# Optimization experiments

Measured on AMD Instinct MI355X. Metric: run time of the kernel, lower is better.

## Reference

```python
import jax, jax.numpy as jnp
import numpy as np

B, N, DIM = 4, 4096, 1024
HEADS, DIM_HEAD = 16, 64
DIM_INNER = HEADS * DIM_HEAD
ATTN_SCALE = 8.0
EPS = 1e-12  # F.normalize default eps


def setup_inputs() -> dict:
    key = jax.random.key(0)
    k1, k2, k3, k4, k5 = jax.random.split(key, 5)
    x = jax.random.normal(k1, (B, N, DIM), dtype=jnp.float32)
    gamma = jnp.ones((DIM,), dtype=jnp.float32)
    # stored as (in, out) so forward is x @ w
    w_qkv = jax.random.normal(k2, (DIM, 3 * DIM_INNER), dtype=jnp.float32) * (DIM ** -0.5)
    temperature = jnp.ones((HEADS, 1, 1), dtype=jnp.float32)
    w_out = jax.random.normal(k3, (DIM_INNER, DIM), dtype=jnp.float32) * (DIM_INNER ** -0.5)
    return {"x": x, "gamma": gamma, "w_qkv": w_qkv, "temperature": temperature, "w_out": w_out}


def _l2norm(t):
    # F.normalize(t, dim=-1): t / max(||t||_2, eps)
    n = jnp.linalg.norm(t, axis=-1, keepdims=True)
    return t / jnp.maximum(n, EPS)


def reference(x, gamma, w_qkv, temperature, w_out):
    b, n, dim = x.shape
    # RMSNorm: F.normalize(x, dim=-1) * sqrt(dim) * gamma
    xn = _l2norm(x) * (dim ** 0.5) * gamma
    # QKV projection -> qkv b h d n
    qkv = (xn @ w_qkv).reshape(b, n, 3, HEADS, DIM_HEAD)
    qkv = qkv.transpose(2, 0, 3, 4, 1)  # (3, b, h, d, n)
    q, k, v = qkv[0], qkv[1], qkv[2]
    # l2-normalize q, k over the sequence (last) axis; temperature-scale q
    q = _l2norm(q) * jnp.exp(temperature)  # temperature: (h,1,1) broadcast
    k = _l2norm(k)
    # cross-covariance attention over the small channel dim d
    sim = jnp.einsum('bhdn,bhen->bhde', q, k) * ATTN_SCALE
    attn = jax.nn.softmax(sim, axis=-1)
    out = jnp.einsum('bhde,bhen->bhdn', attn, v)
    # b h d n -> b n (h d), then out projection
    out = out.transpose(0, 3, 1, 2).reshape(b, n, DIM_INNER)
    return out @ w_out
```

## Files before the change

### kernel.cpp

```cpp
#include <hip/hip_runtime.h>
#include <stdint.h>

typedef unsigned short u16;
typedef unsigned int u32;
typedef __attribute__((ext_vector_type(8))) __bf16 bf16x8;
typedef __attribute__((ext_vector_type(4))) float f32x4;

#define M_TOT 16384
#define DIMX  1024

__device__ __forceinline__ u16 f2b(float f) {
  u32 u = __builtin_bit_cast(u32, f);
  u32 r = (u + 0x7fffu + ((u >> 16) & 1u)) >> 16;
  return (u16)r;
}

__device__ __forceinline__ void gl2lds16(const void* g, void* l) {
  __builtin_amdgcn_global_load_lds((const __attribute__((address_space(1))) void*)g,
                                   (__attribute__((address_space(3))) void*)l,
                                   16, 0, 0);
}

__global__ __launch_bounds__(256) void k_rms(const float* __restrict__ x,
                                             const float* __restrict__ gamma,
                                             u16* __restrict__ xn) {
  int row = blockIdx.x;
  int t = threadIdx.x;
  const float4* xr = (const float4*)(x + (size_t)row * DIMX);
  float4 v = xr[t];
  float ss = v.x * v.x + v.y * v.y + v.z * v.z + v.w * v.w;
#pragma unroll
  for (int o = 32; o > 0; o >>= 1) ss += __shfl_xor(ss, o, 64);
  __shared__ float wss[4];
  int w = t >> 6;
  if ((t & 63) == 0) wss[w] = ss;
  __syncthreads();
  float tot = wss[0] + wss[1] + wss[2] + wss[3];
  float scale = 32.0f / fmaxf(sqrtf(tot), 1e-12f);
  float4 g = ((const float4*)gamma)[t];
  ushort4 o4;
  o4.x = f2b(v.x * scale * g.x);
  o4.y = f2b(v.y * scale * g.y);
  o4.z = f2b(v.z * scale * g.z);
  o4.w = f2b(v.w * scale * g.w);
  ((ushort4*)xn)[(size_t)row * 256 + t] = o4;
}

__global__ __launch_bounds__(256) void k_castT(const float* __restrict__ in,
                                               u16* __restrict__ out, int Rr, int Cc) {
  __shared__ float tile[32][33];
  int c0 = blockIdx.x * 32, r0 = blockIdx.y * 32;
  int tx = threadIdx.x, ty = threadIdx.y;
#pragma unroll
  for (int i = 0; i < 4; i++)
    tile[ty + i * 8][tx] = in[(size_t)(r0 + ty + i * 8) * Cc + c0 + tx];
  __syncthreads();
#pragma unroll
  for (int i = 0; i < 4; i++)
    out[(size_t)(c0 + ty + i * 8) * Rr + r0 + tx] = f2b(tile[tx][ty + i * 8]);
}


template<bool SWAP>
__device__ __forceinline__ f32x4 mf(bf16x8 a, bf16x8 b, f32x4 c) {
  return SWAP ? __builtin_amdgcn_mfma_f32_16x16x32_bf16(b, a, c, 0, 0, 0)
              : __builtin_amdgcn_mfma_f32_16x16x32_bf16(a, b, c, 0, 0, 0);
}

__device__ __forceinline__ void stage_half(const u16* __restrict__ g,
                                           u16* dst, int t, int k0) {
#pragma unroll
  for (int r = 0; r < 2; r++) {
    int chunk = r * 512 + t;
    int row = chunk >> 3;
    int cc = (chunk & 7) ^ (row & 7);
    gl2lds16(g + (size_t)row * 1024 + (k0 + cc * 8),
             dst + (r * 512 + (t >> 6) * 64) * 8);
  }
}

template<bool SWAP>
__device__ __forceinline__ void gemm_core256(const u16* __restrict__ Ag,
                                             const u16* __restrict__ Bg,
                                             u16* lds, int t, f32x4 (&acc)[8][4]) {
  const int lane = t & 63;
  const int r16 = lane & 15, q = lane >> 4;
  const int wr = (t >> 6) >> 2, wc = (t >> 6) & 3;
  const int s0 = (q ^ (r16 & 7)) * 8;
  const int arow = wr * 16 + r16;
  const int brow = wc * 16 + r16;

  stage_half(Ag,              lds + 0 * 8192, t, 0);
  stage_half(Bg,              lds + 2 * 8192, t, 0);
  stage_half(Bg + 128 * 1024, lds + 3 * 8192, t, 0);
  stage_half(Ag + 128 * 1024, lds + 1 * 8192, t, 0);
  asm volatile("s_waitcnt vmcnt(4)" ::: "memory");
  __builtin_amdgcn_s_barrier();

  bf16x8 af[4][2], bl[2][2], bh[2][2];
#pragma unroll 1
  for (int tt = 0; tt < 16; tt++) {
    const int bo = (tt & 1) << 15;
    const int nb = bo ^ 32768;
    const int k1 = ((tt + 1) & 15) << 6;
    const u16* A0 = lds + bo;
    const u16* A1 = lds + bo + 8192;
    const u16* B0 = lds + bo + 16384;
    const u16* B1 = lds + bo + 24576;

#pragma unroll
    for (int i = 0; i < 4; i++) {
      af[i][0] = *(const bf16x8*)(A0 + (i * 32 + arow) * 64 + s0);
      af[i][1] = *(const bf16x8*)(A0 + (i * 32 + arow) * 64 + (s0 ^ 32));
    }
#pragma unroll
    for (int j = 0; j < 2; j++) {
      bl[j][0] = *(const bf16x8*)(B0 + (j * 64 + brow) * 64 + s0);
      bl[j][1] = *(const bf16x8*)(B0 + (j * 64 + brow) * 64 + (s0 ^ 32));
    }
    stage_half(Ag, lds + nb + 0 * 8192, t, k1);
    asm volatile("s_waitcnt lgkmcnt(8)" ::: "memory");
    __builtin_amdgcn_s_barrier();
    asm volatile("s_waitcnt lgkmcnt(0)" ::: "memory");
    __builtin_amdgcn_s_setprio(1);
#pragma unroll
    for (int kq = 0; kq < 2; kq++)
#pragma unroll
      for (int i = 0; i < 4; i++)
#pragma unroll
        for (int j = 0; j < 2; j++)
          acc[i][j] = mf<SWAP>(af[i][kq], bl[j][kq], acc[i][j]);
    __builtin_amdgcn_s_setprio(0);
    asm volatile("s_waitcnt vmcnt(4)" ::: "memory");
    __builtin_amdgcn_s_barrier();

#pragma unroll
    for (int j = 0; j < 2; j++) {
      bh[j][0] = *(const bf16x8*)(B1 + (j * 64 + brow) * 64 + s0);
      bh[j][1] = *(const bf16x8*)(B1 + (j * 64 + brow) * 64 + (s0 ^ 32));
    }
    stage_half(Bg, lds + nb + 2 * 8192, t, k1);
    __builtin_amdgcn_s_barrier();
    asm volatile("s_waitcnt lgkmcnt(0)" ::: "memory");
    __builtin_amdgcn_s_setprio(1);
#pragma unroll
    for (int kq = 0; kq < 2; kq++)
#pragma unroll
      for (int i = 0; i < 4; i++)
#pragma unroll
        for (int j = 0; j < 2; j++)
          acc[i][2 + j] = mf<SWAP>(af[i][kq], bh[j][kq], acc[i][2 + j]);
    __builtin_amdgcn_s_setprio(0);
    asm volatile("s_waitcnt vmcnt(4)" ::: "memory");
    __builtin_amdgcn_s_barrier();

#pragma unroll
    for (int i = 0; i < 4; i++) {
      af[i][0] = *(const bf16x8*)(A1 + (i * 32 + arow) * 64 + s0);
      af[i][1] = *(const bf16x8*)(A1 + (i * 32 + arow) * 64 + (s0 ^ 32));
    }
    stage_half(Bg + 128 * 1024, lds + nb + 3 * 8192, t, k1);
    __builtin_amdgcn_s_barrier();
    asm volatile("s_waitcnt lgkmcnt(0)" ::: "memory");
    __builtin_amdgcn_s_setprio(1);
#pragma unroll
    for (int kq = 0; kq < 2; kq++)
#pragma unroll
      for (int i = 0; i < 4; i++)
#pragma unroll
        for (int j = 0; j < 2; j++)
          acc[4 + i][j] = mf<SWAP>(af[i][kq], bl[j][kq], acc[4 + i][j]);
    __builtin_amdgcn_s_setprio(0);
    __builtin_amdgcn_s_barrier();

    stage_half(Ag + 128 * 1024, lds + nb + 1 * 8192, t, k1);
    __builtin_amdgcn_s_barrier();
    __builtin_amdgcn_s_setprio(1);
#pragma unroll
    for (int kq = 0; kq < 2; kq++)
#pragma unroll
      for (int i = 0; i < 4; i++)
#pragma unroll
        for (int j = 0; j < 2; j++)
          acc[4 + i][2 + j] = mf<SWAP>(af[i][kq], bh[j][kq], acc[4 + i][2 + j]);
    __builtin_amdgcn_s_setprio(0);
    asm volatile("s_waitcnt vmcnt(4)" ::: "memory");
    __builtin_amdgcn_s_barrier();
  }
}

__global__ __launch_bounds__(512, 2) void k_gemm1(const u16* __restrict__ A,
                                                  const u16* __restrict__ Bt,
                                                  u16* __restrict__ qkT,
                                                  u16* __restrict__ vmat,
                                                  float* __restrict__ sumsq) {
  __shared__ u16 lds[8 * 8192];
  int l = blockIdx.x;
  int wg = (l & 7) * 96 + (l >> 3);
  int mt = wg & 63, nt = wg >> 6;
  int m0 = mt * 256, n0 = nt * 256;
  int t = threadIdx.x, lane = t & 63;
  int r16 = lane & 15, q = lane >> 4;
  int wr = (t >> 6) >> 2, wc = (t >> 6) & 3;
  f32x4 acc[8][4] = {};
  if (n0 < 2048) {
    gemm_core256<false>(A + (size_t)m0 * 1024, Bt + (size_t)n0 * 1024, lds, t, acc);
    int b = m0 >> 12;
#pragma unroll
    for (int j = 0; j < 4; j++) {
      int c = n0 + j * 64 + wc * 16 + r16;
      float colss = 0.f;
#pragma unroll
      for (int i = 0; i < 8; i++) {
        f32x4 a = acc[i][j];
        colss += a.x * a.x + a.y * a.y + a.z * a.z + a.w * a.w;
        int m = m0 + i * 32 + wr * 16 + q * 4;
        ushort4 o4;
        o4.x = f2b(a.x); o4.y = f2b(a.y); o4.z = f2b(a.z); o4.w = f2b(a.w);
        *(ushort4*)(qkT + (size_t)c * M_TOT + m) = o4;
      }
      colss += __shfl_xor(colss, 16, 64);
      colss += __shfl_xor(colss, 32, 64);
      if (lane < 16) atomicAdd(&sumsq[b * 2048 + c], colss);
    }
  } else {
    gemm_core256<true>(A + (size_t)m0 * 1024, Bt + (size_t)n0 * 1024, lds, t, acc);
    int vc0 = n0 - 2048;
#pragma unroll
    for (int i = 0; i < 8; i++) {
      int m = m0 + i * 32 + wr * 16 + r16;
#pragma unroll
      for (int j = 0; j < 4; j++) {
        int c = vc0 + j * 64 + wc * 16 + q * 4;
        f32x4 a = acc[i][j];
        ushort4 o4;
        o4.x = f2b(a.x); o4.y = f2b(a.y); o4.z = f2b(a.z); o4.w = f2b(a.w);
        *(ushort4*)(vmat + (size_t)m * 1024 + c) = o4;
      }
    }
  }
}

__global__ __launch_bounds__(256) void k_attn_s(const u16* __restrict__ qkT,
                                                float* __restrict__ Spart) {
  int g = blockIdx.x, split = blockIdx.y;
  int t = threadIdx.x, lane = t & 63, w = t >> 6;
  int bh = g * 4 + w;
  int b = bh >> 4, h = bh & 15;
  int r16 = lane & 15, q = lane >> 4;
  const u16* qbase = qkT + (size_t)(h * 64) * M_TOT + b * 4096;
  const u16* kbase = qkT + (size_t)(1024 + h * 64) * M_TOT + b * 4096;
  f32x4 acc[4][4] = {};
#pragma unroll
  for (int it = 0; it < 8; it++) {
    int kk = split * 256 + it * 32 + q * 8;
    bf16x8 af[4], bfr[4];
#pragma unroll
    for (int i = 0; i < 4; i++) af[i] = *(const bf16x8*)(qbase + (size_t)(i * 16 + r16) * M_TOT + kk);
#pragma unroll
    for (int j = 0; j < 4; j++) bfr[j] = *(const bf16x8*)(kbase + (size_t)(j * 16 + r16) * M_TOT + kk);
#pragma unroll
    for (int i = 0; i < 4; i++)
#pragma unroll
      for (int j = 0; j < 4; j++)
        acc[i][j] = __builtin_amdgcn_mfma_f32_16x16x32_bf16(bfr[j], af[i], acc[i][j], 0, 0, 0);
  }
  float* Sp = Spart + ((size_t)split * 64 + bh) * 4096;
#pragma unroll
  for (int i = 0; i < 4; i++) {
    int d = i * 16 + r16;
#pragma unroll
    for (int j = 0; j < 4; j++) {
      int e = j * 16 + q * 4;
      *(f32x4*)(Sp + d * 64 + e) = acc[i][j];
    }
  }
}

__global__ __launch_bounds__(64) void k_softmax(const float* __restrict__ Spart,
                                                const float* __restrict__ sumsq,
                                                const float* __restrict__ temp,
                                                u16* __restrict__ PT) {
  int bh = blockIdx.x;
  int b = bh >> 4, h = bh & 15;
  int d = threadIdx.x;
  __shared__ float rnk[64];
  rnk[d] = 1.0f / fmaxf(sqrtf(sumsq[b * 2048 + 1024 + h * 64 + d]), 1e-12f);
  __syncthreads();
  float nq = sqrtf(sumsq[b * 2048 + h * 64 + d]);
  float qs = 8.0f * __expf(temp[h]) / fmaxf(nq, 1e-12f);
  const float* Sp = Spart + (size_t)bh * 4096 + d * 64;
  float vals[64];
#pragma unroll
  for (int e = 0; e < 64; e += 4) {
    f32x4 v = {};
#pragma unroll
    for (int s = 0; s < 16; s++)
      v += *(const f32x4*)(Sp + (size_t)s * 64 * 4096 + e);
    vals[e + 0] = v.x; vals[e + 1] = v.y; vals[e + 2] = v.z; vals[e + 3] = v.w;
  }
  float mx = -3.0e38f;
#pragma unroll
  for (int e = 0; e < 64; e++) {
    float v = vals[e] * qs * rnk[e];
    vals[e] = v;
    mx = fmaxf(mx, v);
  }
  float sum = 0.f;
#pragma unroll
  for (int e = 0; e < 64; e++) {
    float v = __expf(vals[e] - mx);
    vals[e] = v;
    sum += v;
  }
  float inv = 1.0f / sum;
#pragma unroll
  for (int e = 0; e < 64; e++)
    PT[((size_t)bh * 64 + e) * 64 + d] = f2b(vals[e] * inv);
}

__global__ __launch_bounds__(256) void k_m(const u16* __restrict__ woT,
                                           const u16* __restrict__ PT,
                                           u16* __restrict__ MT) {
  int bh = blockIdx.x;
  int b = bh >> 4, h = bh & 15;
  int o0 = blockIdx.y * 128;
  int t = threadIdx.x, lane = t & 63, w = t >> 6;
  int r16 = lane & 15, q = lane >> 4;
  const u16* pbase = PT + (size_t)bh * 4096;
  f32x4 acc[2][4] = {};
#pragma unroll
  for (int ks = 0; ks < 2; ks++) {
    int kk = ks * 32 + q * 8;
    bf16x8 af[2], bfr[4];
#pragma unroll
    for (int i = 0; i < 2; i++)
      af[i] = *(const bf16x8*)(woT + (size_t)(o0 + w * 32 + i * 16 + r16) * 1024 + h * 64 + kk);
#pragma unroll
    for (int j = 0; j < 4; j++)
      bfr[j] = *(const bf16x8*)(pbase + (size_t)(j * 16 + r16) * 64 + kk);
#pragma unroll
    for (int i = 0; i < 2; i++)
#pragma unroll
      for (int j = 0; j < 4; j++)
        acc[i][j] = __builtin_amdgcn_mfma_f32_16x16x32_bf16(af[i], bfr[j], acc[i][j], 0, 0, 0);
  }
  u16* dst = MT + (size_t)b * 1024 * 1024;
#pragma unroll
  for (int i = 0; i < 2; i++) {
    int o = o0 + w * 32 + i * 16 + q * 4;
#pragma unroll
    for (int j = 0; j < 4; j++) {
      int e = h * 64 + j * 16 + r16;
      f32x4 a = acc[i][j];
      dst[(size_t)(o + 0) * 1024 + e] = f2b(a.x);
      dst[(size_t)(o + 1) * 1024 + e] = f2b(a.y);
      dst[(size_t)(o + 2) * 1024 + e] = f2b(a.z);
      dst[(size_t)(o + 3) * 1024 + e] = f2b(a.w);
    }
  }
}

__global__ __launch_bounds__(512, 2) void k_gemm2(const u16* __restrict__ A,
                                                  const u16* __restrict__ Bt,
                                                  float* __restrict__ C) {
  __shared__ u16 lds[8 * 8192];
  int l = blockIdx.x;
  int wg = (l & 7) * 32 + (l >> 3);
  int mt = wg & 63, nt = wg >> 6;
  int m0 = mt * 256, n0 = nt * 256;
  int b = m0 >> 12;
  const u16* Bb = Bt + (size_t)b * 1024 * 1024;
  int t = threadIdx.x, lane = t & 63;
  int r16 = lane & 15, q = lane >> 4;
  int wr = (t >> 6) >> 2, wc = (t >> 6) & 3;
  f32x4 acc[8][4] = {};
  gemm_core256<true>(A + (size_t)m0 * 1024, Bb + (size_t)n0 * 1024, lds, t, acc);
#pragma unroll
  for (int i = 0; i < 8; i++) {
    int m = m0 + i * 32 + wr * 16 + r16;
#pragma unroll
    for (int j = 0; j < 4; j++) {
      int c = n0 + j * 64 + wc * 16 + q * 4;
      *(f32x4*)(C + (size_t)m * 1024 + c) = acc[i][j];
    }
  }
}

extern "C" void kernel_launch(void* const* d_in, const int* in_sizes, int n_in,
                              void* d_out, int out_size, void* d_ws, size_t ws_size,
                              hipStream_t stream) {
  const float* x     = (const float*)d_in[0];
  const float* gamma = (const float*)d_in[1];
  const float* wqkv  = (const float*)d_in[2];
  const float* temp  = (const float*)d_in[3];
  const float* wout  = (const float*)d_in[4];
  float* out = (float*)d_out;

  char* ws = (char*)d_ws;
  size_t off = 0;
  u16* xn = (u16*)(ws + off);    off += (size_t)M_TOT * 1024 * 2;
  u16* wqT = (u16*)(ws + off);   off += (size_t)3072 * 1024 * 2;
  u16* woT = (u16*)(ws + off);   off += (size_t)1024 * 1024 * 2;
  u16* qkT = (u16*)(ws + off);   off += (size_t)2048 * M_TOT * 2;
  u16* vmat = (u16*)(ws + off);  off += (size_t)M_TOT * 1024 * 2;
  float* sumsq = (float*)(ws + off); off += (size_t)4 * 2048 * 4;
  u16* PT = (u16*)(ws + off);    off += (size_t)64 * 64 * 64 * 2;
  u16* MT = (u16*)(ws + off);    off += (size_t)4 * 1024 * 1024 * 2;

  float* Spart = (float*)xn;

  hipMemsetAsync((void*)sumsq, 0, (size_t)4 * 2048 * 4, stream);

  k_rms<<<16384, 256, 0, stream>>>(x, gamma, xn);
  dim3 cb(32, 8);
  k_castT<<<dim3(3072 / 32, 1024 / 32), cb, 0, stream>>>(wqkv, wqT, 1024, 3072);
  k_castT<<<dim3(1024 / 32, 1024 / 32), cb, 0, stream>>>(wout, woT, 1024, 1024);
  k_gemm1<<<768, 512, 0, stream>>>(xn, wqT, qkT, vmat, sumsq);
  k_attn_s<<<dim3(16, 16), 256, 0, stream>>>(qkT, Spart);
  k_softmax<<<64, 64, 0, stream>>>(Spart, sumsq, temp, PT);
  k_m<<<dim3(64, 8), 256, 0, stream>>>(woT, PT, MT);
  k_gemm2<<<1024 / 4, 512, 0, stream>>>(vmat, MT, out);
}
```

Baseline: 338.0 us.

## Drop intra-iteration barriers in GEMM core and remap tiles per XCD

Removes several workgroup barriers and explicit LDS waitcnts between the async stage issue and the MFMA phases in the 256x256 GEMM main loop. One barrier with a vmcnt wait is kept per phase boundary. This cuts synchronisation stalls so waves can overlap LDS reads, staging and MFMA more freely. Both GEMMs also change their block-to-tile mapping so each XCD gets 8 consecutive M tiles, which should improve L2 reuse of the A operand. Fewer barriers risk LDS read/write races if the remaining waits do not cover every hazard.

```diff
diff --git a/kernel.cpp b/kernel.cpp
--- a/kernel.cpp
+++ b/kernel.cpp
@@ -119,9 +119,6 @@
       bl[j][1] = *(const bf16x8*)(B0 + (j * 64 + brow) * 64 + (s0 ^ 32));
     }
     stage_half(Ag, lds + nb + 0 * 8192, t, k1);
-    asm volatile("s_waitcnt lgkmcnt(8)" ::: "memory");
-    __builtin_amdgcn_s_barrier();
-    asm volatile("s_waitcnt lgkmcnt(0)" ::: "memory");
     __builtin_amdgcn_s_setprio(1);
 #pragma unroll
     for (int kq = 0; kq < 2; kq++)
@@ -140,8 +137,6 @@
       bh[j][1] = *(const bf16x8*)(B1 + (j * 64 + brow) * 64 + (s0 ^ 32));
     }
     stage_half(Bg, lds + nb + 2 * 8192, t, k1);
-    __builtin_amdgcn_s_barrier();
-    asm volatile("s_waitcnt lgkmcnt(0)" ::: "memory");
     __builtin_amdgcn_s_setprio(1);
 #pragma unroll
     for (int kq = 0; kq < 2; kq++)
@@ -160,8 +155,6 @@
       af[i][1] = *(const bf16x8*)(A1 + (i * 32 + arow) * 64 + (s0 ^ 32));
     }
     stage_half(Bg + 128 * 1024, lds + nb + 3 * 8192, t, k1);
-    __builtin_amdgcn_s_barrier();
-    asm volatile("s_waitcnt lgkmcnt(0)" ::: "memory");
     __builtin_amdgcn_s_setprio(1);
 #pragma unroll
     for (int kq = 0; kq < 2; kq++)
@@ -174,7 +167,6 @@
     __builtin_amdgcn_s_barrier();
 
     stage_half(Ag + 128 * 1024, lds + nb + 1 * 8192, t, k1);
-    __builtin_amdgcn_s_barrier();
     __builtin_amdgcn_s_setprio(1);
 #pragma unroll
     for (int kq = 0; kq < 2; kq++)
@@ -196,8 +188,9 @@
                                                   float* __restrict__ sumsq) {
   __shared__ u16 lds[8 * 8192];
   int l = blockIdx.x;
-  int wg = (l & 7) * 96 + (l >> 3);
-  int mt = wg & 63, nt = wg >> 6;
+  int xcd = l & 7, c = l >> 3;
+  int mt = xcd * 8 + (c & 7);
+  int nt = c >> 3;
   int m0 = mt * 256, n0 = nt * 256;
   int t = threadIdx.x, lane = t & 63;
   int r16 = lane & 15, q = lane >> 4;
@@ -208,7 +201,7 @@
     int b = m0 >> 12;
 #pragma unroll
     for (int j = 0; j < 4; j++) {
-      int c = n0 + j * 64 + wc * 16 + r16;
+      int cc = n0 + j * 64 + wc * 16 + r16;
       float colss = 0.f;
 #pragma unroll
       for (int i = 0; i < 8; i++) {
@@ -217,11 +210,11 @@
         int m = m0 + i * 32 + wr * 16 + q * 4;
         ushort4 o4;
         o4.x = f2b(a.x); o4.y = f2b(a.y); o4.z = f2b(a.z); o4.w = f2b(a.w);
-        *(ushort4*)(qkT + (size_t)c * M_TOT + m) = o4;
+        *(ushort4*)(qkT + (size_t)cc * M_TOT + m) = o4;
       }
       colss += __shfl_xor(colss, 16, 64);
       colss += __shfl_xor(colss, 32, 64);
-      if (lane < 16) atomicAdd(&sumsq[b * 2048 + c], colss);
+      if (lane < 16) atomicAdd(&sumsq[b * 2048 + cc], colss);
     }
   } else {
     gemm_core256<true>(A + (size_t)m0 * 1024, Bt + (size_t)n0 * 1024, lds, t, acc);
@@ -231,11 +224,11 @@
       int m = m0 + i * 32 + wr * 16 + r16;
 #pragma unroll
       for (int j = 0; j < 4; j++) {
-        int c = vc0 + j * 64 + wc * 16 + q * 4;
+        int cc = vc0 + j * 64 + wc * 16 + q * 4;
         f32x4 a = acc[i][j];
         ushort4 o4;
         o4.x = f2b(a.x); o4.y = f2b(a.y); o4.z = f2b(a.z); o4.w = f2b(a.w);
-        *(ushort4*)(vmat + (size_t)m * 1024 + c) = o4;
+        *(ushort4*)(vmat + (size_t)m * 1024 + cc) = o4;
       }
     }
   }
@@ -366,8 +359,9 @@
                                                   float* __restrict__ C) {
   __shared__ u16 lds[8 * 8192];
   int l = blockIdx.x;
-  int wg = (l & 7) * 32 + (l >> 3);
-  int mt = wg & 63, nt = wg >> 6;
+  int xcd = l & 7, c = l >> 3;
+  int mt = xcd * 8 + (c & 7);
+  int nt = c >> 3;
   int m0 = mt * 256, n0 = nt * 256;
   int b = m0 >> 12;
   const u16* Bb = Bt + (size_t)b * 1024 * 1024;
@@ -381,8 +375,8 @@
     int m = m0 + i * 32 + wr * 16 + r16;
 #pragma unroll
     for (int j = 0; j < 4; j++) {
-      int c = n0 + j * 64 + wc * 16 + q * 4;
-      *(f32x4*)(C + (size_t)m * 1024 + c) = acc[i][j];
+      int cc = n0 + j * 64 + wc * 16 + q * 4;
+      *(f32x4*)(C + (size_t)m * 1024 + cc) = acc[i][j];
     }
   }
 }
```

Result: faster. 324.7 us (-3.9%).
